# Optimization experiments

Hardware: AMD Instinct MI355X
Metric: run time of the kernel (lower is better)

Reference implementation:

```python
import jax, jax.numpy as jnp
import numpy as np

B, T, C, H, L, V = 2, 1024, 768, 12, 12, 50257
D = C // H  # head size = 64
EPS = 1e-5


def _layer_norm(x, w, b):
    m = x.mean(-1, keepdims=True)
    v = x.var(-1, keepdims=True)
    return (x - m) * jax.lax.rsqrt(v + EPS) * w + b


def setup_inputs() -> dict:
    key = jax.random.key(0)
    ks = jax.random.split(key, 8)
    std = 0.02
    res_std = 0.02 * (2 * L) ** -0.5  # NANOGPT_SCALE_INIT
    rn = lambda k, shape, s: jax.random.normal(k, shape, jnp.float32) * s
    return dict(
        idx=jax.random.randint(ks[0], (B, T), 0, V),
        wte=rn(ks[1], (V, C), std),
        wpe=rn(ks[2], (T, C), std),
        ln1_w=jnp.ones((L, C), jnp.float32), ln1_b=jnp.zeros((L, C), jnp.float32),
        qkv_w=rn(ks[3], (L, C, 3 * C), std), qkv_b=jnp.zeros((L, 3 * C), jnp.float32),
        proj_w=rn(ks[4], (L, C, C), res_std), proj_b=jnp.zeros((L, C), jnp.float32),
        ln2_w=jnp.ones((L, C), jnp.float32), ln2_b=jnp.zeros((L, C), jnp.float32),
        fc_w=rn(ks[5], (L, C, 4 * C), std), fc_b=jnp.zeros((L, 4 * C), jnp.float32),
        fco_w=rn(ks[6], (L, 4 * C, C), res_std), fco_b=jnp.zeros((L, C), jnp.float32),
        lnf_w=jnp.ones((C,), jnp.float32), lnf_b=jnp.zeros((C,), jnp.float32),
    )


def reference(idx, wte, wpe, ln1_w, ln1_b, qkv_w, qkv_b, proj_w, proj_b,
              ln2_w, ln2_b, fc_w, fc_b, fco_w, fco_b, lnf_w, lnf_b):
    x = wte[idx] + wpe[:T]  # [B, T, C] tok + pos emb
    mask = jnp.tril(jnp.ones((T, T), bool))  # causal
    scale = 1.0 / np.sqrt(D).astype(np.float32)

    def block(x, p):
        l1w, l1b, qw, qb, pw, pb, l2w, l2b, fw, fb, fow, fob = p
        h = _layer_norm(x, l1w, l1b)
        qkv = h @ qw + qb  # [B, T, 3C]
        q, k, v = jnp.split(qkv, 3, axis=-1)
        q = q.reshape(B, T, H, D)
        k = k.reshape(B, T, H, D)
        v = v.reshape(B, T, H, D)
        att = jnp.einsum('bqhd,bkhd->bhqk', q, k) * scale
        att = jnp.where(mask, att, -jnp.inf)
        att = jax.nn.softmax(att, axis=-1)
        y = jnp.einsum('bhqk,bkhd->bqhd', att, v).reshape(B, T, C)
        x = x + y @ pw + pb
        h2 = _layer_norm(x, l2w, l2b)
        x = x + jax.nn.gelu(h2 @ fw + fb, approximate=True) @ fow + fob
        return x, None

    x, _ = jax.lax.scan(block, x, (ln1_w, ln1_b, qkv_w, qkv_b, proj_w, proj_b,
                                   ln2_w, ln2_b, fc_w, fc_b, fco_w, fco_b))
    x = _layer_norm(x, lnf_w, lnf_b)
    logits = x @ wte.T  # tied lm_head
    return logits
```

## Files before the change

### kernel.cpp

```cpp
#include <hip/hip_runtime.h>
#include <cmath>
#include <cstdint>

#define T_SEQ 1024
#define NH 12
#define NL 12
#define NV 50257
#define CD 768
#define M_ROWS 2048

typedef __bf16 bf16_t;
typedef __bf16 bf16x4 __attribute__((ext_vector_type(4)));
typedef __bf16 bf16x8 __attribute__((ext_vector_type(8)));
typedef float f32x4 __attribute__((ext_vector_type(4)));

__device__ __forceinline__ void gload16(const bf16_t* g, bf16_t* l) {
  __builtin_amdgcn_global_load_lds(
      (const __attribute__((address_space(1))) void*)g,
      (__attribute__((address_space(3))) void*)l, 16, 0, 0);
}

__global__ __launch_bounds__(256) void embed_k(const int* __restrict__ idx,
    const float* __restrict__ wte, const float* __restrict__ wpe,
    float* __restrict__ x) {
  int m = blockIdx.x;
  int t = m & (T_SEQ - 1);
  int tok = idx[m];
  const float* a = wte + (size_t)tok * CD;
  const float* p = wpe + (size_t)t * CD;
  float* xr = x + (size_t)m * CD;
  int c = threadIdx.x;
  xr[c]       = a[c]       + p[c];
  xr[c + 256] = a[c + 256] + p[c + 256];
  xr[c + 512] = a[c + 512] + p[c + 512];
}

__global__ __launch_bounds__(256) void cvt_k(const float* __restrict__ in,
    bf16_t* __restrict__ out, int n4) {
  int i = blockIdx.x * 256 + threadIdx.x;
  if (i < n4) {
    float4 v = ((const float4*)in)[i];
    bf16_t* o = out + (size_t)i * 4;
    o[0] = (bf16_t)v.x; o[1] = (bf16_t)v.y;
    o[2] = (bf16_t)v.z; o[3] = (bf16_t)v.w;
  }
}

__global__ __launch_bounds__(256) void transcvt_k(const float* __restrict__ W0,
    bf16_t* __restrict__ WT0, int K, int N) {
  const float* W = W0 + (size_t)blockIdx.z * K * N;
  bf16_t* WT = WT0 + (size_t)blockIdx.z * N * K;
  __shared__ float tl[32][33];
  int k0 = blockIdx.y * 32, n0 = blockIdx.x * 32;
  int j = threadIdx.x & 31, i0 = threadIdx.x >> 5;
  #pragma unroll
  for (int i = i0; i < 32; i += 8) tl[i][j] = W[(size_t)(k0 + i) * N + n0 + j];
  __syncthreads();
  #pragma unroll
  for (int i = i0; i < 32; i += 8)
    WT[(size_t)(n0 + i) * K + k0 + j] = (bf16_t)tl[j][i];
}

__global__ __launch_bounds__(192) void ln_k(const float* __restrict__ x,
    const float* __restrict__ w, const float* __restrict__ bi,
    bf16_t* __restrict__ out) {
  int row = blockIdx.x;
  int t = threadIdx.x;
  float4 v = ((const float4*)(x + (size_t)row * CD))[t];
  float s  = (v.x + v.y) + (v.z + v.w);
  float ss = (v.x * v.x + v.y * v.y) + (v.z * v.z + v.w * v.w);
  #pragma unroll
  for (int o = 1; o < 64; o <<= 1) { s += __shfl_xor(s, o); ss += __shfl_xor(ss, o); }
  __shared__ float sh[6];
  int wid = t >> 6, lane = t & 63;
  if (lane == 0) { sh[wid] = s; sh[3 + wid] = ss; }
  __syncthreads();
  s  = sh[0] + sh[1] + sh[2];
  ss = sh[3] + sh[4] + sh[5];
  float mean = s * (1.f / CD);
  float var  = ss * (1.f / CD) - mean * mean;
  float rs = rsqrtf(var + 1e-5f);
  float4 w4 = ((const float4*)w)[t];
  float4 b4 = ((const float4*)bi)[t];
  bf16x4 o;
  o[0] = (bf16_t)((v.x - mean) * rs * w4.x + b4.x);
  o[1] = (bf16_t)((v.y - mean) * rs * w4.y + b4.y);
  o[2] = (bf16_t)((v.z - mean) * rs * w4.z + b4.z);
  o[3] = (bf16_t)((v.w - mean) * rs * w4.w + b4.w);
  *(bf16x4*)(out + (size_t)row * CD + t * 4) = o;
}

template <int BM, int BN, int BK, int EPI, bool FUSEVT, int XSWZ>
__global__ __launch_bounds__(256) void gemm_bt(
    const bf16_t* __restrict__ A,
    const bf16_t* __restrict__ BT,
    const float* __restrict__ bias,
    const float* __restrict__ resid,
    void* __restrict__ out_p,
    bf16_t* __restrict__ vt,
    int Mdim, int Ndim, int Kdim) {
  constexpr int MR = BM / 32, NR = BN / 32;
  constexpr int KS = BK / 32;
  constexpr int LPW = (BM + BN) * BK / 2048;
  __shared__ __align__(1024) bf16_t As[3][BM * BK];
  __shared__ __align__(1024) bf16_t Bs[3][BN * BK];
  const int t = threadIdx.x;
  const int wid = t >> 6, lane = t & 63;
  const int wm = wid >> 1, wn = wid & 1;
  int bx = blockIdx.x, by = blockIdx.y;
  if (XSWZ == 1) {
    int gx = gridDim.x;
    int lin = by * gx + bx;
    int cpx = (gx * gridDim.y) >> 3;
    int swz = (lin & 7) * cpx + (lin >> 3);
    bx = swz % gx; by = swz / gx;
  }
  const int m0 = by * BM, n0 = bx * BN;
  const int l15 = lane & 15, lhi = lane >> 4;

  auto stage = [&](int bi, int kt) {
    if (BK == 32) {
      const int srow = lane >> 2, schk = lane & 3;
      #pragma unroll
      for (int i = 0; i < BM / 64; ++i) {
        int rbase = wid * (BM / 4) + i * 16;
        int r = rbase + srow;
        int c = schk ^ ((r >> 1) & 3);
        gload16(A + (size_t)(m0 + r) * Kdim + kt + c * 8, &As[bi][rbase * 32]);
      }
      #pragma unroll
      for (int i = 0; i < BN / 64; ++i) {
        int rbase = wid * (BN / 4) + i * 16;
        int r = rbase + srow;
        int nr = n0 + r; if (nr >= Ndim) nr = Ndim - 1;
        int c = schk ^ ((r >> 1) & 3);
        gload16(BT + (size_t)nr * Kdim + kt + c * 8, &Bs[bi][rbase * 32]);
      }
    } else {
      const int srow = lane >> 3, schk = lane & 7;
      #pragma unroll
      for (int i = 0; i < BM / 32; ++i) {
        int rbase = wid * (BM / 4) + i * 8;
        int r = rbase + srow;
        int c = schk ^ (r & 7);
        gload16(A + (size_t)(m0 + r) * Kdim + kt + c * 8, &As[bi][rbase * 64]);
      }
      #pragma unroll
      for (int i = 0; i < BN / 32; ++i) {
        int rbase = wid * (BN / 4) + i * 8;
        int r = rbase + srow;
        int nr = n0 + r; if (nr >= Ndim) nr = Ndim - 1;
        int c = schk ^ (r & 7);
        gload16(BT + (size_t)nr * Kdim + kt + c * 8, &Bs[bi][rbase * 64]);
      }
    }
  };

  f32x4 acc[MR][NR] = {};
  const int NT = Kdim / BK;

  stage(0, 0);
  if (NT > 1) stage(1, BK);
  for (int tt = 0; tt < NT; ++tt) {
    if (tt < NT - 1) asm volatile("s_waitcnt vmcnt(%0)" :: "i"(LPW) : "memory");
    else             asm volatile("s_waitcnt vmcnt(0)" ::: "memory");
    __builtin_amdgcn_sched_barrier(0);
    __builtin_amdgcn_s_barrier();
    __builtin_amdgcn_sched_barrier(0);

    const bf16_t* Ab = As[tt % 3];
    const bf16_t* Bb = Bs[tt % 3];
    bf16x8 af[KS][MR], bfr[KS][NR];
    #pragma unroll
    for (int ks = 0; ks < KS; ++ks) {
      #pragma unroll
      for (int mm = 0; mm < MR; ++mm) {
        int ra = wm * (BM / 2) + mm * 16 + l15;
        int ch = (BK == 32) ? ((lhi ^ (ra >> 1)) & 3) : ((ks * 4 + lhi) ^ (ra & 7));
        af[ks][mm] = *(const bf16x8*)&Ab[ra * BK + ch * 8];
      }
      #pragma unroll
      for (int nn = 0; nn < NR; ++nn) {
        int rb = wn * (BN / 2) + nn * 16 + l15;
        int ch = (BK == 32) ? ((lhi ^ (rb >> 1)) & 3) : ((ks * 4 + lhi) ^ (rb & 7));
        bfr[ks][nn] = *(const bf16x8*)&Bb[rb * BK + ch * 8];
      }
    }
    if (tt + 2 < NT) stage((tt + 2) % 3, (tt + 2) * BK);

    __builtin_amdgcn_s_setprio(1);
    #pragma unroll
    for (int ks = 0; ks < KS; ++ks)
      #pragma unroll
      for (int mm = 0; mm < MR; ++mm)
        #pragma unroll
        for (int nn = 0; nn < NR; ++nn)
          acc[mm][nn] = __builtin_amdgcn_mfma_f32_16x16x32_bf16(
              af[ks][mm], bfr[ks][nn], acc[mm][nn], 0, 0, 0);
    __builtin_amdgcn_s_setprio(0);

    __builtin_amdgcn_sched_barrier(0);
    __builtin_amdgcn_s_barrier();
    __builtin_amdgcn_sched_barrier(0);
  }

  bf16_t* ob = (bf16_t*)out_p;
  float*  of = (float*)out_p;
  const int row0 = m0 + wm * (BM / 2);
  const int col0 = n0 + wn * (BN / 2);
  #pragma unroll
  for (int mm = 0; mm < MR; ++mm) {
    #pragma unroll
    for (int nn = 0; nn < NR; ++nn) {
      int col = col0 + nn * 16 + l15;
      if (col >= Ndim) continue;
      float bv = (EPI != 3) ? bias[col] : 0.f;
      if (EPI == 0) {
        bf16_t vv[4];
        #pragma unroll
        for (int r = 0; r < 4; ++r) {
          int row = row0 + mm * 16 + lhi * 4 + r;
          float v = acc[mm][nn][r] + bv;
          vv[r] = (bf16_t)v;
          ob[(size_t)row * Ndim + col] = vv[r];
        }
        if (FUSEVT && col >= 2 * CD) {
          int h = (col - 2 * CD) >> 6;
          int d = (col - 2 * CD) & 63;
          int brow = row0 + mm * 16 + lhi * 4;
          int bh = (brow >> 10) * NH + h;
          int tt0 = brow & (T_SEQ - 1);
          *(bf16x4*)&vt[((size_t)bh * 64 + d) * T_SEQ + tt0] = *(const bf16x4*)vv;
        }
      } else {
        #pragma unroll
        for (int r = 0; r < 4; ++r) {
          int row = row0 + mm * 16 + lhi * 4 + r;
          float v = acc[mm][nn][r] + bv;
          size_t o = (size_t)row * Ndim + col;
          if (EPI == 1) {
            float u = v + 0.044715f * v * v * v;
            float w2 = 1.59576912f * u;
            v = v / (1.f + __expf(-w2));
            ob[o] = (bf16_t)v;
          } else if (EPI == 2) {
            of[o] = resid[o] + v;
          } else {
            of[o] = v;
          }
        }
      }
    }
  }
}

#define LMH_GY 197
__global__ __launch_bounds__(512, 2) void gemm_lm(
    const bf16_t* __restrict__ A,
    const bf16_t* __restrict__ BT,
    float* __restrict__ out) {
  __shared__ __align__(1024) bf16_t As[4][256 * 32];
  __shared__ __align__(1024) bf16_t Bs[4][256 * 32];
  const int t = threadIdx.x;
  const int wid = t >> 6, lane = t & 63;
  const int wr = wid >> 2, wc = wid & 3;
  const int l15 = lane & 15, lhi = lane >> 4;
  const int srow = lane >> 2;
  const int schk = lane & 3;

  int lin = blockIdx.x;
  int swz = (lin & 7) * LMH_GY + (lin >> 3);
  const int m0 = (swz & 7) * 256;
  const int n0 = (swz >> 3) * 256;

  auto stage = [&](int bi, int kt) {
    #pragma unroll
    for (int hf = 0; hf < 2; ++hf) {
      int rb = hf * 128 + wid * 16;
      int r = rb + srow;
      int c = schk ^ ((r >> 1) & 3);
      gload16(A + (size_t)(m0 + r) * CD + kt * 32 + c * 8, &As[bi][rb * 32]);
    }
    #pragma unroll
    for (int hf = 0; hf < 2; ++hf) {
      int rb = hf * 128 + wid * 16;
      int r = rb + srow;
      int nr = n0 + r; if (nr >= NV) nr = NV - 1;
      int c = schk ^ ((r >> 1) & 3);
      gload16(BT + (size_t)nr * CD + kt * 32 + c * 8, &Bs[bi][rb * 32]);
    }
  };

  f32x4 acc[8][4] = {};
  const int NT = CD / 32;

  stage(0, 0); stage(1, 1); stage(2, 2);
  for (int tt = 0; tt < NT; ++tt) {
    if (tt < NT - 2)       asm volatile("s_waitcnt vmcnt(8)" ::: "memory");
    else if (tt == NT - 2) asm volatile("s_waitcnt vmcnt(4)" ::: "memory");
    else                   asm volatile("s_waitcnt vmcnt(0)" ::: "memory");
    __builtin_amdgcn_sched_barrier(0);
    __builtin_amdgcn_s_barrier();
    __builtin_amdgcn_sched_barrier(0);

    const bf16_t* Ab = As[tt & 3];
    const bf16_t* Bb = Bs[tt & 3];
    bf16x8 af[8], bfr[4];
    #pragma unroll
    for (int mm = 0; mm < 8; ++mm) {
      int ra = wr * 128 + mm * 16 + l15;
      af[mm] = *(const bf16x8*)&Ab[ra * 32 + ((lhi ^ (ra >> 1)) & 3) * 8];
    }
    #pragma unroll
    for (int nn = 0; nn < 4; ++nn) {
      int rb = wc * 64 + nn * 16 + l15;
      bfr[nn] = *(const bf16x8*)&Bb[rb * 32 + ((lhi ^ (rb >> 1)) & 3) * 8];
    }
    if (tt + 3 < NT) stage((tt + 3) & 3, tt + 3);

    __builtin_amdgcn_s_setprio(1);
    #pragma unroll
    for (int mm = 0; mm < 8; ++mm)
      #pragma unroll
      for (int nn = 0; nn < 4; ++nn)
        acc[mm][nn] = __builtin_amdgcn_mfma_f32_16x16x32_bf16(af[mm], bfr[nn], acc[mm][nn], 0, 0, 0);
    __builtin_amdgcn_s_setprio(0);

    __builtin_amdgcn_sched_barrier(0);
    __builtin_amdgcn_s_barrier();
    __builtin_amdgcn_sched_barrier(0);
  }

  const int row0 = m0 + wr * 128;
  const int col0 = n0 + wc * 64;
  #pragma unroll
  for (int mm = 0; mm < 8; ++mm) {
    #pragma unroll
    for (int nn = 0; nn < 4; ++nn) {
      int col = col0 + nn * 16 + l15;
      if (col >= NV) continue;
      #pragma unroll
      for (int r = 0; r < 4; ++r)
        out[(size_t)(row0 + mm * 16 + lhi * 4 + r) * NV + col] = acc[mm][nn][r];
    }
  }
}

__global__ __launch_bounds__(64) void attn_k(const bf16_t* __restrict__ qkv,
                                             const bf16_t* __restrict__ VT,
                                             bf16_t* __restrict__ y) {
  __shared__ __align__(16) bf16_t Ps[16 * 40];
  const int lane = threadIdx.x;
  const int gw = blockIdx.x;
  const int qi = gw & 63;
  const int bh = gw >> 6;
  const int h = bh % NH, b = bh / NH;
  const bf16_t* Qbase = qkv + (size_t)b * T_SEQ * (3 * CD) + h * 64;
  const bf16_t* Kbase = Qbase + CD;
  const bf16_t* Vt = VT + (size_t)bh * 64 * T_SEQ;

  const int l15 = lane & 15, lhi = lane >> 4;
  const int q0 = qi * 16;

  bf16x8 aq[2];
  #pragma unroll
  for (int c = 0; c < 2; ++c)
    aq[c] = *(const bf16x8*)(Qbase + (size_t)(q0 + l15) * (3 * CD) + c * 32 + lhi * 8);

  f32x4 acc[4] = {};
  float m_[4], l_[4];
  #pragma unroll
  for (int r = 0; r < 4; ++r) { m_[r] = -INFINITY; l_[r] = 0.f; }

  const int qrow = q0 + lhi * 4;
  const int nt = (q0 + 47) / 32;
  for (int kt = 0; kt < nt; ++kt) {
    const int k0 = kt * 32;
    f32x4 s[2] = {};
    #pragma unroll
    for (int c = 0; c < 2; ++c) {
      #pragma unroll
      for (int kc = 0; kc < 2; ++kc) {
        bf16x8 bk = *(const bf16x8*)(Kbase + (size_t)(k0 + kc * 16 + l15) * (3 * CD) + c * 32 + lhi * 8);
        s[kc] = __builtin_amdgcn_mfma_f32_16x16x32_bf16(aq[c], bk, s[kc], 0, 0, 0);
      }
    }
    float mx[4];
    #pragma unroll
    for (int r = 0; r < 4; ++r) mx[r] = -INFINITY;
    #pragma unroll
    for (int kc = 0; kc < 2; ++kc) {
      const int kcol = k0 + kc * 16 + l15;
      #pragma unroll
      for (int r = 0; r < 4; ++r) {
        float sv = (kcol <= qrow + r) ? s[kc][r] * 0.125f : -INFINITY;
        s[kc][r] = sv;
        mx[r] = fmaxf(mx[r], sv);
      }
    }
    #pragma unroll
    for (int r = 0; r < 4; ++r) {
      mx[r] = fmaxf(mx[r], __shfl_xor(mx[r], 1));
      mx[r] = fmaxf(mx[r], __shfl_xor(mx[r], 2));
      mx[r] = fmaxf(mx[r], __shfl_xor(mx[r], 4));
      mx[r] = fmaxf(mx[r], __shfl_xor(mx[r], 8));
    }
    float al[4], rs[4];
    #pragma unroll
    for (int r = 0; r < 4; ++r) {
      float mn = fmaxf(m_[r], mx[r]);
      al[r] = __expf(m_[r] - mn);
      m_[r] = mn;
      float p0 = __expf(s[0][r] - mn);
      float p1 = __expf(s[1][r] - mn);
      s[0][r] = p0; s[1][r] = p1;
      rs[r] = p0 + p1;
    }
    #pragma unroll
    for (int r = 0; r < 4; ++r) {
      rs[r] += __shfl_xor(rs[r], 1);
      rs[r] += __shfl_xor(rs[r], 2);
      rs[r] += __shfl_xor(rs[r], 4);
      rs[r] += __shfl_xor(rs[r], 8);
      l_[r] = l_[r] * al[r] + rs[r];
    }
    #pragma unroll
    for (int dt = 0; dt < 4; ++dt)
      #pragma unroll
      for (int r = 0; r < 4; ++r) acc[dt][r] *= al[r];
    #pragma unroll
    for (int kc = 0; kc < 2; ++kc)
      #pragma unroll
      for (int r = 0; r < 4; ++r)
        Ps[(lhi * 4 + r) * 40 + kc * 16 + l15] = (bf16_t)s[kc][r];
    bf16x8 pa = *(const bf16x8*)&Ps[l15 * 40 + lhi * 8];
    #pragma unroll
    for (int dt = 0; dt < 4; ++dt) {
      bf16x8 bv = *(const bf16x8*)(Vt + (size_t)(dt * 16 + l15) * T_SEQ + k0 + lhi * 8);
      acc[dt] = __builtin_amdgcn_mfma_f32_16x16x32_bf16(pa, bv, acc[dt], 0, 0, 0);
    }
  }
  #pragma unroll
  for (int dt = 0; dt < 4; ++dt) {
    #pragma unroll
    for (int r = 0; r < 4; ++r)
      y[(size_t)(b * T_SEQ + q0 + lhi * 4 + r) * CD + h * 64 + dt * 16 + l15] =
          (bf16_t)(acc[dt][r] / l_[r]);
  }
}

extern "C" void kernel_launch(void* const* d_in, const int* in_sizes, int n_in,
                              void* d_out, int out_size, void* d_ws, size_t ws_size,
                              hipStream_t stream) {
  const int*   idx   = (const int*)d_in[0];
  const float* wte   = (const float*)d_in[1];
  const float* wpe   = (const float*)d_in[2];
  const float* ln1w  = (const float*)d_in[3];
  const float* ln1b  = (const float*)d_in[4];
  const float* qkvw  = (const float*)d_in[5];
  const float* qkvb  = (const float*)d_in[6];
  const float* projw = (const float*)d_in[7];
  const float* projb = (const float*)d_in[8];
  const float* ln2w  = (const float*)d_in[9];
  const float* ln2b  = (const float*)d_in[10];
  const float* fcw   = (const float*)d_in[11];
  const float* fcb   = (const float*)d_in[12];
  const float* fcow  = (const float*)d_in[13];
  const float* fcob  = (const float*)d_in[14];
  const float* lnfw  = (const float*)d_in[15];
  const float* lnfb  = (const float*)d_in[16];
  float* out = (float*)d_out;

  char* w = (char*)d_ws;
  auto alloc = [&](size_t bytes) {
    char* p = w; w += (bytes + 255) & ~(size_t)255; return p;
  };
  float*  x     = (float*)alloc((size_t)M_ROWS * CD * 4);
  float*  x2    = (float*)alloc((size_t)M_ROWS * CD * 4);
  bf16_t* hb    = (bf16_t*)alloc((size_t)M_ROWS * CD * 2);
  bf16_t* qkvB  = (bf16_t*)alloc((size_t)M_ROWS * 3 * CD * 2);
  bf16_t* yb    = (bf16_t*)alloc((size_t)M_ROWS * CD * 2);
  bf16_t* fca   = (bf16_t*)alloc((size_t)M_ROWS * 4 * CD * 2);
  bf16_t* VT    = (bf16_t*)alloc((size_t)2 * NH * 64 * T_SEQ * 2);
  bf16_t* wteB  = (bf16_t*)alloc((size_t)NV * CD * 2);
  bf16_t* wqT_s = (bf16_t*)alloc((size_t)3 * CD * CD * 2);
  bf16_t* wpT_s = (bf16_t*)alloc((size_t)CD * CD * 2);
  bf16_t* wfT_s = (bf16_t*)alloc((size_t)4 * CD * CD * 2);
  bf16_t* woT_s = (bf16_t*)alloc((size_t)CD * 4 * CD * 2);
  const size_t qkvSz = (size_t)3 * CD * CD, prSz = (size_t)CD * CD;
  const size_t fcSz  = (size_t)4 * CD * CD, foSz = (size_t)CD * 4 * CD;
  bf16_t* wqT_b = (bf16_t*)alloc(NL * qkvSz * 2);
  bf16_t* wpT_b = (bf16_t*)alloc(NL * prSz * 2);
  bf16_t* wfT_b = (bf16_t*)alloc(NL * fcSz * 2);
  bf16_t* woT_b = (bf16_t*)alloc(NL * foSz * 2);
  const bool big = (size_t)(w - (char*)d_ws) <= ws_size;

  embed_k<<<M_ROWS, 256, 0, stream>>>(idx, wte, wpe, x);
  {
    int n4 = NV * CD / 4;
    cvt_k<<<(n4 + 255) / 256, 256, 0, stream>>>(wte, wteB, n4);
  }
  if (big) {
    transcvt_k<<<dim3(3 * CD / 32, CD / 32, NL), 256, 0, stream>>>(qkvw,  wqT_b, CD, 3 * CD);
    transcvt_k<<<dim3(CD / 32, CD / 32, NL),     256, 0, stream>>>(projw, wpT_b, CD, CD);
    transcvt_k<<<dim3(4 * CD / 32, CD / 32, NL), 256, 0, stream>>>(fcw,   wfT_b, CD, 4 * CD);
    transcvt_k<<<dim3(CD / 32, 4 * CD / 32, NL), 256, 0, stream>>>(fcow,  woT_b, 4 * CD, CD);
  }

  for (int l = 0; l < NL; ++l) {
    bf16_t *wqT, *wpT, *wfT, *woT;
    if (big) {
      wqT = wqT_b + (size_t)l * qkvSz; wpT = wpT_b + (size_t)l * prSz;
      wfT = wfT_b + (size_t)l * fcSz;  woT = woT_b + (size_t)l * foSz;
    } else {
      wqT = wqT_s; wpT = wpT_s; wfT = wfT_s; woT = woT_s;
      transcvt_k<<<dim3(3 * CD / 32, CD / 32, 1), 256, 0, stream>>>(qkvw  + (size_t)l * CD * 3 * CD, wqT, CD, 3 * CD);
      transcvt_k<<<dim3(CD / 32, CD / 32, 1),     256, 0, stream>>>(projw + (size_t)l * CD * CD,     wpT, CD, CD);
      transcvt_k<<<dim3(4 * CD / 32, CD / 32, 1), 256, 0, stream>>>(fcw   + (size_t)l * CD * 4 * CD, wfT, CD, 4 * CD);
      transcvt_k<<<dim3(CD / 32, 4 * CD / 32, 1), 256, 0, stream>>>(fcow  + (size_t)l * 4 * CD * CD, woT, 4 * CD, CD);
    }

    ln_k<<<M_ROWS, 192, 0, stream>>>(x, ln1w + l * CD, ln1b + l * CD, hb);
    gemm_bt<64, 128, 32, 0, true, 1><<<dim3(3 * CD / 128, M_ROWS / 64), 256, 0, stream>>>(
        hb, wqT, qkvb + l * 3 * CD, nullptr, qkvB, VT, M_ROWS, 3 * CD, CD);
    attn_k<<<2 * NH * 64, 64, 0, stream>>>(qkvB, VT, yb);
    gemm_bt<64, 64, 64, 2, false, 1><<<dim3(CD / 64, M_ROWS / 64), 256, 0, stream>>>(
        yb, wpT, projb + l * CD, x, x2, nullptr, M_ROWS, CD, CD);
    ln_k<<<M_ROWS, 192, 0, stream>>>(x2, ln2w + l * CD, ln2b + l * CD, hb);
    gemm_bt<64, 128, 32, 1, false, 1><<<dim3(4 * CD / 128, M_ROWS / 64), 256, 0, stream>>>(
        hb, wfT, fcb + l * 4 * CD, nullptr, fca, nullptr, M_ROWS, 4 * CD, CD);
    gemm_bt<64, 64, 64, 2, false, 1><<<dim3(CD / 64, M_ROWS / 64), 256, 0, stream>>>(
        fca, woT, fcob + l * CD, x2, x, nullptr, M_ROWS, CD, 4 * CD);
  }

  ln_k<<<M_ROWS, 192, 0, stream>>>(x, lnfw, lnfb, hb);
  gemm_lm<<<8 * LMH_GY, 512, 0, stream>>>(hb, wteB, out);
}
```

Before: 2.060 ms.

## Restructure LM-head GEMM to 4 waves with 128x128 warp tiles and triple buffering

```diff
diff --git a/kernel.cpp b/kernel.cpp
--- a/kernel.cpp
+++ b/kernel.cpp
@@ -255,15 +255,15 @@
 }
 
 #define LMH_GY 197
-__global__ __launch_bounds__(512, 2) void gemm_lm(
+__global__ __launch_bounds__(256, 1) void gemm_lmW(
     const bf16_t* __restrict__ A,
     const bf16_t* __restrict__ BT,
     float* __restrict__ out) {
-  __shared__ __align__(1024) bf16_t As[4][256 * 32];
-  __shared__ __align__(1024) bf16_t Bs[4][256 * 32];
+  __shared__ __align__(1024) bf16_t As[3][256 * 32];
+  __shared__ __align__(1024) bf16_t Bs[3][256 * 32];
   const int t = threadIdx.x;
   const int wid = t >> 6, lane = t & 63;
-  const int wr = wid >> 2, wc = wid & 3;
+  const int wm = wid >> 1, wn = wid & 1;
   const int l15 = lane & 15, lhi = lane >> 4;
   const int srow = lane >> 2;
   const int schk = lane & 3;
@@ -275,54 +275,53 @@
 
   auto stage = [&](int bi, int kt) {
     #pragma unroll
-    for (int hf = 0; hf < 2; ++hf) {
-      int rb = hf * 128 + wid * 16;
-      int r = rb + srow;
+    for (int i = 0; i < 4; ++i) {
+      int rbase = wid * 64 + i * 16;
+      int r = rbase + srow;
       int c = schk ^ ((r >> 1) & 3);
-      gload16(A + (size_t)(m0 + r) * CD + kt * 32 + c * 8, &As[bi][rb * 32]);
-    }
-    #pragma unroll
-    for (int hf = 0; hf < 2; ++hf) {
-      int rb = hf * 128 + wid * 16;
-      int r = rb + srow;
+      gload16(A + (size_t)(m0 + r) * CD + kt * 32 + c * 8, &As[bi][rbase * 32]);
+    }
+    #pragma unroll
+    for (int i = 0; i < 4; ++i) {
+      int rbase = wid * 64 + i * 16;
+      int r = rbase + srow;
       int nr = n0 + r; if (nr >= NV) nr = NV - 1;
       int c = schk ^ ((r >> 1) & 3);
-      gload16(BT + (size_t)nr * CD + kt * 32 + c * 8, &Bs[bi][rb * 32]);
+      gload16(BT + (size_t)nr * CD + kt * 32 + c * 8, &Bs[bi][rbase * 32]);
     }
   };
 
-  f32x4 acc[8][4] = {};
+  f32x4 acc[8][8] = {};
   const int NT = CD / 32;
 
-  stage(0, 0); stage(1, 1); stage(2, 2);
+  stage(0, 0); stage(1, 1);
   for (int tt = 0; tt < NT; ++tt) {
-    if (tt < NT - 2)       asm volatile("s_waitcnt vmcnt(8)" ::: "memory");
-    else if (tt == NT - 2) asm volatile("s_waitcnt vmcnt(4)" ::: "memory");
-    else                   asm volatile("s_waitcnt vmcnt(0)" ::: "memory");
+    if (tt < NT - 1) asm volatile("s_waitcnt vmcnt(8)" ::: "memory");
+    else             asm volatile("s_waitcnt vmcnt(0)" ::: "memory");
     __builtin_amdgcn_sched_barrier(0);
     __builtin_amdgcn_s_barrier();
     __builtin_amdgcn_sched_barrier(0);
 
-    const bf16_t* Ab = As[tt & 3];
-    const bf16_t* Bb = Bs[tt & 3];
-    bf16x8 af[8], bfr[4];
+    const bf16_t* Ab = As[tt % 3];
+    const bf16_t* Bb = Bs[tt % 3];
+    bf16x8 af[8], bfr[8];
     #pragma unroll
     for (int mm = 0; mm < 8; ++mm) {
-      int ra = wr * 128 + mm * 16 + l15;
+      int ra = wm * 128 + mm * 16 + l15;
       af[mm] = *(const bf16x8*)&Ab[ra * 32 + ((lhi ^ (ra >> 1)) & 3) * 8];
     }
     #pragma unroll
-    for (int nn = 0; nn < 4; ++nn) {
-      int rb = wc * 64 + nn * 16 + l15;
+    for (int nn = 0; nn < 8; ++nn) {
+      int rb = wn * 128 + nn * 16 + l15;
       bfr[nn] = *(const bf16x8*)&Bb[rb * 32 + ((lhi ^ (rb >> 1)) & 3) * 8];
     }
-    if (tt + 3 < NT) stage((tt + 3) & 3, tt + 3);
+    if (tt + 2 < NT) stage((tt + 2) % 3, tt + 2);
 
     __builtin_amdgcn_s_setprio(1);
     #pragma unroll
     for (int mm = 0; mm < 8; ++mm)
       #pragma unroll
-      for (int nn = 0; nn < 4; ++nn)
+      for (int nn = 0; nn < 8; ++nn)
         acc[mm][nn] = __builtin_amdgcn_mfma_f32_16x16x32_bf16(af[mm], bfr[nn], acc[mm][nn], 0, 0, 0);
     __builtin_amdgcn_s_setprio(0);
 
@@ -331,12 +330,12 @@
     __builtin_amdgcn_sched_barrier(0);
   }
 
-  const int row0 = m0 + wr * 128;
-  const int col0 = n0 + wc * 64;
+  const int row0 = m0 + wm * 128;
+  const int col0 = n0 + wn * 128;
   #pragma unroll
   for (int mm = 0; mm < 8; ++mm) {
     #pragma unroll
-    for (int nn = 0; nn < 4; ++nn) {
+    for (int nn = 0; nn < 8; ++nn) {
       int col = col0 + nn * 16 + l15;
       if (col >= NV) continue;
       #pragma unroll
@@ -534,5 +533,5 @@
   }
 
   ln_k<<<M_ROWS, 192, 0, stream>>>(x, lnfw, lnfb, hb);
-  gemm_lm<<<8 * LMH_GY, 512, 0, stream>>>(hb, wteB, out);
-}
+  gemm_lmW<<<8 * LMH_GY, 256, 0, stream>>>(hb, wteB, out);
+}
```

Measured after the change: 2.074 ms. Within noise of the previous version (+0.7%).
